# Kernel tuning notes

Measured on AMD Instinct MI355X. Metric: run time of the kernel, lower is better.

## Reference

```python
import jax, jax.numpy as jnp
import numpy as np

R = 2          # candidate_radius
TEMP = 0.1     # temperature
MIN_E = 3
MAX_E = 8      # max_edges_per_node
EPS = 1e-6


def _neighbors(H, W, r):
    # grid neighbor indices (N,K) and relative positions (K,2), clamped at borders
    ys, xs = np.meshgrid(np.arange(H), np.arange(W), indexing='ij')
    idx_grid = ys * W + xs
    nbrs, rel = [], []
    for dy in range(-r, r + 1):
        for dx in range(-r, r + 1):
            if dy == 0 and dx == 0:
                continue
            ny = np.clip(ys + dy, 0, H - 1)
            nx = np.clip(xs + dx, 0, W - 1)
            nbrs.append(idx_grid[ny, nx].ravel())
            rel.append([dx / r, dy / r])
    return jnp.asarray(np.stack(nbrs, 1)), jnp.asarray(np.array(rel, np.float32))


def setup_inputs() -> dict:
    key = jax.random.key(0)
    ks = jax.random.split(key, 12)
    B, C, H, W = 2, 64, 128, 128
    hid = 64
    ein = 2 * C + 2  # edge scorer input dim
    s = 0.05
    return {
        'x':  jax.random.normal(ks[0], (B, C, H, W), jnp.float32),
        'W1': jax.random.normal(ks[1], (hid, ein), jnp.float32) * s,
        'b1': jnp.zeros((hid,), jnp.float32),
        'W2': jax.random.normal(ks[2], (hid // 2, hid), jnp.float32) * s,
        'b2': jnp.zeros((hid // 2,), jnp.float32),
        'W3': jax.random.normal(ks[3], (1, hid // 2), jnp.float32) * s,
        'b3': jnp.zeros((1,), jnp.float32),
        'thr': jnp.asarray(0.0, jnp.float32),
        'Wm': jax.random.normal(ks[4], (C, C), jnp.float32) * s,
        'bm': jnp.zeros((C,), jnp.float32),
        'Wo': jax.random.normal(ks[5], (C, C), jnp.float32) * s,
        'bo': jnp.zeros((C,), jnp.float32),
    }


def reference(x, W1, b1, W2, b2, W3, b3, thr, Wm, bm, Wo, bo):
    B, C, H, W = x.shape
    N = H * W
    nbr, rel = _neighbors(H, W, R)          # (N,K), (K,2)
    K = nbr.shape[1]

    nodes = x.transpose(0, 2, 3, 1).reshape(B, N, C)   # (B,N,C)
    h_tgt = jnp.take(nodes, nbr, axis=1)               # (B,N,K,C) gather neighbors

    # edge scorer layer1: split W1 over [h_src | h_tgt | rel_pos] to avoid (B,N,K,2C+2) concat
    z_src = nodes @ W1[:, :C].T                        # (B,N,hid)
    z_tgt = h_tgt @ W1[:, C:2 * C].T                   # (B,N,K,hid)
    z_pos = rel @ W1[:, 2 * C:].T                      # (K,hid)
    h1 = jax.nn.relu(z_src[:, :, None, :] + z_tgt + z_pos[None, None] + b1)
    h2 = jax.nn.relu(h1 @ W2.T + b2)
    edge_scores = jax.nn.sigmoid((h2 @ W3.T + b3)[..., 0])   # (B,N,K)

    thr_v = jax.nn.sigmoid(thr)
    keep_prob = jax.nn.sigmoid((edge_scores - thr_v) / TEMP)
    mask_thr = edge_scores >= thr_v
    counts = mask_thr.sum(axis=2)                       # (B,N)

    def topk_mask(k):
        _, idx = jax.lax.top_k(edge_scores, k)          # (B,N,k)
        return jax.nn.one_hot(idx, K, dtype=jnp.float32).sum(-2) > 0

    m_max = topk_mask(min(MAX_E, K))
    m_min = topk_mask(min(MIN_E, K))
    use_max = (counts > MAX_E)[..., None]
    use_min = (counts < MIN_E)[..., None]
    use_t = ~use_max & ~use_min
    final_mask = (use_max & m_max) | (use_min & m_min) | (use_t & mask_thr)

    msgs = jax.nn.relu(h_tgt @ Wm.T + bm)               # (B,N,K,C)
    w = (edge_scores * keep_prob * final_mask.astype(edge_scores.dtype))[..., None]
    agg = (msgs * w).sum(axis=2) / (w.sum(axis=2) + EPS)  # (B,N,C)

    out = nodes + agg @ Wo.T + bo
    return out.reshape(B, H, W, C).transpose(0, 3, 1, 2)
```

## Files before the change

kernel.cpp:

```cpp
#include <hip/hip_runtime.h>
#include <hip/hip_bf16.h>
#include <math.h>

#define NNODES 16384
#define KE 24

typedef float f32x4 __attribute__((ext_vector_type(4)));
typedef unsigned u32x4 __attribute__((ext_vector_type(4)));
typedef __fp16 half2_t __attribute__((ext_vector_type(2)));
typedef _Float16 half8_t __attribute__((ext_vector_type(8)));

union fragcast { u32x4 u; half8_t h; half2_t h2[4]; };

__global__ void aux_k(const float* __restrict__ W1, const float* __restrict__ Wm,
                      float* __restrict__ zpos, float* __restrict__ wt)
{
    int t = threadIdx.x;
    for (int idx = t; idx < KE * 64; idx += 256) {
        int k = idx >> 6, h = idx & 63;
        int kk = k + (k >= 12 ? 1 : 0);
        int q5 = (kk * 52) >> 8;
        int dy = q5 - 2;
        int dx = kk - 5 * q5 - 2;
        zpos[idx] = W1[h * 130 + 128] * (dx * 0.5f)
                  + W1[h * 130 + 129] * (dy * 0.5f);
    }
    for (int idx = t; idx < 3 * 64 * 64; idx += 256) {
        int mat = idx >> 12;
        int r = idx & 4095;
        int c = r >> 6, h = r & 63;
        float v = (mat == 0) ? W1[h * 130 + c]
                : (mat == 1) ? W1[h * 130 + 64 + c]
                             : Wm[h * 64 + c];
        wt[idx] = v;
    }
}

__global__ __launch_bounds__(256) void precompute_k(
    const float* __restrict__ x, const float* __restrict__ wt,
    const float* __restrict__ b1, const float* __restrict__ bm,
    float* __restrict__ zsrc, float* __restrict__ ztgt, float* __restrict__ msg)
{
    __shared__ float xt[64][128];
    __shared__ float wl[64][64];
    const int t = threadIdx.x;
    const int mat = blockIdx.x >> 8;
    const int tile = blockIdx.x & 255;
    const int n0 = tile * 128;
    const int b = n0 >> 14;
    const int nl0 = n0 & (NNODES - 1);
    const float* xb = x + (size_t)b * 64 * NNODES + nl0;

    #pragma unroll
    for (int r = 0; r < 8; ++r) {
        int idx = r * 256 + t;
        int c = idx >> 5, j4 = idx & 31;
        float4 v = *(const float4*)(xb + (size_t)c * NNODES + j4 * 4);
        *(float4*)&xt[c][j4 * 4] = v;
    }
    #pragma unroll
    for (int r = 0; r < 4; ++r) {
        int idx = r * 256 + t;
        ((float4*)&wl[0][0])[idx] = ((const float4*)(wt + mat * 4096))[idx];
    }
    __syncthreads();

    const int i = t >> 5;
    const int j = t & 31;

    float acc[8][4];
    #pragma unroll
    for (int a = 0; a < 8; ++a)
        #pragma unroll
        for (int bb = 0; bb < 4; ++bb) acc[a][bb] = 0.f;

    #pragma unroll 4
    for (int c = 0; c < 64; ++c) {
        float4 w0 = *(const float4*)&wl[c][i * 8];
        float4 w1 = *(const float4*)&wl[c][i * 8 + 4];
        float4 x0 = *(const float4*)&xt[c][j * 4];
        float wv[8] = {w0.x, w0.y, w0.z, w0.w, w1.x, w1.y, w1.z, w1.w};
        float xv[4] = {x0.x, x0.y, x0.z, x0.w};
        #pragma unroll
        for (int a = 0; a < 8; ++a)
            #pragma unroll
            for (int bb = 0; bb < 4; ++bb)
                acc[a][bb] = fmaf(wv[a], xv[bb], acc[a][bb]);
    }

    #pragma unroll
    for (int a = 0; a < 8; ++a) {
        float bv = (mat == 0) ? b1[i * 8 + a] : (mat == 2) ? bm[i * 8 + a] : 0.f;
        #pragma unroll
        for (int bb = 0; bb < 4; ++bb) {
            float v = acc[a][bb] + bv;
            acc[a][bb] = (mat == 2) ? fmaxf(v, 0.f) : v;
        }
    }

    float* dst = (mat == 0) ? zsrc : (mat == 1) ? ztgt : msg;
    #pragma unroll
    for (int bb = 0; bb < 4; ++bb) {
        float* o = dst + (size_t)(n0 + j * 4 + bb) * 64 + i * 8;
        *(float4*)o       = make_float4(acc[0][bb], acc[1][bb], acc[2][bb], acc[3][bb]);
        *(float4*)(o + 4) = make_float4(acc[4][bb], acc[5][bb], acc[6][bb], acc[7][bb]);
    }
}

__global__ __launch_bounds__(256, 3) void score_k(
    const float* __restrict__ zsrc, const float* __restrict__ ztgt,
    const float* __restrict__ zpos, const float* __restrict__ W2,
    const float* __restrict__ b2, const float* __restrict__ W3,
    const float* __restrict__ b3, float* __restrict__ scores)
{
    __shared__ fragcast fraglds[64 * 13];
    __shared__ float zpl[24 * 68];

    const int t = threadIdx.x;
    const int l = t & 63;
    const int lcol = l & 15;
    const int lgrp = l >> 4;
    const int w = t >> 6;
    const int wave = blockIdx.x * 4 + w;

    #pragma unroll
    for (int r = 0; r < 6; ++r) {
        int idx = r * 256 + t;
        zpl[(idx >> 6) * 68 + (idx & 63)] = zpos[idx];
    }
    {
        const int jt = w >> 1, kt = w & 1;
        fragcast fh, fl;
        const float* wr = W2 + (size_t)(jt * 16 + lcol) * 64 + kt * 32 + lgrp * 8;
        #pragma unroll
        for (int d = 0; d < 4; ++d) {
            float e0 = wr[2 * d] * 64.f;
            float e1 = wr[2 * d + 1] * 64.f;
            half2_t hh = __builtin_amdgcn_cvt_pkrtz(e0, e1);
            float r0 = e0 - (float)hh[0];
            float r1 = e1 - (float)hh[1];
            fh.h2[d] = hh;
            fl.h2[d] = __builtin_amdgcn_cvt_pkrtz(r0, r1);
        }
        fraglds[l * 13 + 0 + jt * 2 + kt] = fh;
        fraglds[l * 13 + 4 + jt * 2 + kt] = fl;
    }
    __syncthreads();

    const fragcast* fb = &fraglds[l * 13];
    const f32x4 b2l0 = *(const f32x4*)(b2 + lgrp * 4);
    const f32x4 b2l1 = *(const f32x4*)(b2 + 16 + lgrp * 4);
    const f32x4 w3l0 = *(const f32x4*)(W3 + lgrp * 4);
    const f32x4 w3l1 = *(const f32x4*)(W3 + 16 + lgrp * 4);
    const float b3s = b3[0];

    const int node0 = wave * 2;

    #pragma unroll
    for (int Mt = 0; Mt < 3; ++Mt) {
        const int ke = Mt * 16 + lcol;
        const int nsel = (ke >= 24) ? 1 : 0;
        const int node = node0 + nsel;
        const int k = ke - 24 * nsel;
        const int bb = node >> 14;
        const int nl = node & (NNODES - 1);
        const int yy = nl >> 7, xx = nl & 127;
        const int kk = k + (k >= 12 ? 1 : 0);
        const int q5 = (kk * 52) >> 8;
        const int dy = q5 - 2, dx = kk - 5 * q5 - 2;
        const int ny = min(max(yy + dy, 0), 127);
        const int nx = min(max(xx + dx, 0), 127);
        const int nbn = (bb << 14) + (ny << 7) + nx;

        const float* zs = zsrc + (size_t)node * 64 + lgrp * 8;
        const float* zt = ztgt + (size_t)nbn * 64 + lgrp * 8;
        const float* zp = &zpl[k * 68 + lgrp * 8];

        f32x4 ac0A = {0.f,0.f,0.f,0.f}, ac0B = {0.f,0.f,0.f,0.f};
        f32x4 ac1A = {0.f,0.f,0.f,0.f}, ac1B = {0.f,0.f,0.f,0.f};

        #pragma unroll
        for (int kt = 0; kt < 2; ++kt) {
            const int o = kt * 32;
            float4 a0 = *(const float4*)(zs + o);
            float4 a1 = *(const float4*)(zs + o + 4);
            float4 t0 = *(const float4*)(zt + o);
            float4 t1 = *(const float4*)(zt + o + 4);
            float4 p0 = *(const float4*)(zp + o);
            float4 p1 = *(const float4*)(zp + o + 4);
            float v[8];
            v[0] = fmaxf(a0.x + t0.x + p0.x, 0.f);
            v[1] = fmaxf(a0.y + t0.y + p0.y, 0.f);
            v[2] = fmaxf(a0.z + t0.z + p0.z, 0.f);
            v[3] = fmaxf(a0.w + t0.w + p0.w, 0.f);
            v[4] = fmaxf(a1.x + t1.x + p1.x, 0.f);
            v[5] = fmaxf(a1.y + t1.y + p1.y, 0.f);
            v[6] = fmaxf(a1.z + t1.z + p1.z, 0.f);
            v[7] = fmaxf(a1.w + t1.w + p1.w, 0.f);

            fragcast Bh, Bl;
            #pragma unroll
            for (int d = 0; d < 4; ++d) {
                float e0 = v[2 * d], e1 = v[2 * d + 1];
                half2_t hh = __builtin_amdgcn_cvt_pkrtz(e0, e1);
                float r0 = e0 - (float)hh[0];
                float r1 = e1 - (float)hh[1];
                Bh.h2[d] = hh;
                Bl.h2[d] = __builtin_amdgcn_cvt_pkrtz(r0, r1);
            }

            ac0A = __builtin_amdgcn_mfma_f32_16x16x32_f16(fb[0 + kt].h, Bh.h, ac0A, 0, 0, 0);
            ac1A = __builtin_amdgcn_mfma_f32_16x16x32_f16(fb[2 + kt].h, Bh.h, ac1A, 0, 0, 0);
            ac0B = __builtin_amdgcn_mfma_f32_16x16x32_f16(fb[4 + kt].h, Bh.h, ac0B, 0, 0, 0);
            ac1B = __builtin_amdgcn_mfma_f32_16x16x32_f16(fb[6 + kt].h, Bh.h, ac1B, 0, 0, 0);
            ac0B = __builtin_amdgcn_mfma_f32_16x16x32_f16(fb[0 + kt].h, Bl.h, ac0B, 0, 0, 0);
            ac1B = __builtin_amdgcn_mfma_f32_16x16x32_f16(fb[2 + kt].h, Bl.h, ac1B, 0, 0, 0);
        }

        const f32x4 s0 = ac0A + ac0B;
        const f32x4 s1 = ac1A + ac1B;
        float sacc = 0.f;
        #pragma unroll
        for (int q = 0; q < 4; ++q) {
            sacc = fmaf(fmaxf(fmaf(s0[q], 0.015625f, b2l0[q]), 0.f), w3l0[q], sacc);
            sacc = fmaf(fmaxf(fmaf(s1[q], 0.015625f, b2l1[q]), 0.f), w3l1[q], sacc);
        }
        sacc += __shfl_xor(sacc, 16);
        sacc += __shfl_xor(sacc, 32);
        float sig = 1.f / (1.f + expf(-(sacc + b3s)));
        if (l < 16)
            scores[(size_t)node0 * 24 + Mt * 16 + l] = sig;
    }
}

__global__ __launch_bounds__(256) void agg_k(
    const float* __restrict__ x, const float* __restrict__ scores,
    const float* __restrict__ msg, const float* __restrict__ Wo,
    const float* __restrict__ bo, const float* __restrict__ thrp,
    float* __restrict__ out)
{
    __shared__ float sc[768];
    __shared__ float wl[768];
    __shared__ float sumw[32];
    __shared__ float aggL[32][64];
    __shared__ float ot[64][33];

    const int t = threadIdx.x;
    const int n0 = blockIdx.x * 32;
    const int b = n0 >> 14;
    const int nl0 = n0 & (NNODES - 1);
    const float thr_v = 1.f / (1.f + expf(-thrp[0]));

    #pragma unroll
    for (int rep = 0; rep < 3; ++rep)
        sc[rep * 256 + t] = scores[(size_t)n0 * 24 + rep * 256 + t];
    __syncthreads();

    #pragma unroll
    for (int rep = 0; rep < 3; ++rep) {
        int e = rep * 256 + t;
        int nl = (int)(((unsigned)(e >> 3) * 171u) >> 9);
        int k = e - nl * 24;
        float s_e = sc[e];
        int rank = 0, cnt = 0;
        #pragma unroll
        for (int j = 0; j < 24; ++j) {
            float sj = sc[nl * 24 + j];
            rank += (sj > s_e || (sj == s_e && j < k)) ? 1 : 0;
            cnt  += (sj >= thr_v) ? 1 : 0;
        }
        bool mask = (cnt > 8) ? (rank < 8)
                  : ((cnt < 3) ? (rank < 3) : (s_e >= thr_v));
        float keep = 1.f / (1.f + expf(-(s_e - thr_v) * 10.f));
        wl[e] = mask ? s_e * keep : 0.f;
    }
    __syncthreads();

    if (t < 32) {
        float s = 0.f;
        #pragma unroll
        for (int k = 0; k < 24; ++k) s += wl[t * 24 + k];
        sumw[t] = s + 1e-6f;
    }
    __syncthreads();

    const int lane = t & 63;
    const int g4 = t >> 6;

    #pragma unroll
    for (int it = 0; it < 8; ++it) {
        int nl = g4 + it * 4;
        int nn = nl0 + nl;
        int yy = nn >> 7, xx = nn & 127;
        float acc = 0.f;
        #pragma unroll
        for (int k = 0; k < 24; ++k) {
            int kk = k + (k >= 12 ? 1 : 0);
            int q5 = (kk * 52) >> 8;
            int dy = q5 - 2, dx = kk - 5 * q5 - 2;
            int ny = min(max(yy + dy, 0), 127);
            int nx = min(max(xx + dx, 0), 127);
            int nb = (b << 14) + (ny << 7) + nx;
            acc = fmaf(wl[nl * 24 + k], msg[(size_t)nb * 64 + lane], acc);
        }
        aggL[nl][lane] = acc / sumw[nl];
    }

    float4 wo[16];
    #pragma unroll
    for (int c4 = 0; c4 < 16; ++c4) wo[c4] = ((const float4*)Wo)[lane * 16 + c4];
    __syncthreads();

    #pragma unroll
    for (int it = 0; it < 8; ++it) {
        int nl = g4 + it * 4;
        const float4* ar = (const float4*)aggL[nl];
        float a0 = 0.f, a1 = 0.f, a2 = 0.f, a3 = 0.f;
        #pragma unroll
        for (int c4 = 0; c4 < 16; ++c4) {
            float4 wv = wo[c4];
            float4 av = ar[c4];
            a0 = fmaf(av.x, wv.x, a0);
            a1 = fmaf(av.y, wv.y, a1);
            a2 = fmaf(av.z, wv.z, a2);
            a3 = fmaf(av.w, wv.w, a3);
        }
        float v = (a0 + a1) + (a2 + a3) + bo[lane]
                + x[(size_t)b * 64 * NNODES + (size_t)lane * NNODES + nl0 + nl];
        ot[lane][nl] = v;
    }
    __syncthreads();

    #pragma unroll
    for (int rep = 0; rep < 2; ++rep) {
        int idx = rep * 256 + t;
        int o = idx >> 3, p = idx & 7;
        float4 v = make_float4(ot[o][4 * p + 0], ot[o][4 * p + 1],
                               ot[o][4 * p + 2], ot[o][4 * p + 3]);
        *(float4*)(out + (size_t)b * 64 * NNODES + (size_t)o * NNODES + nl0 + 4 * p) = v;
    }
}

extern "C" void kernel_launch(void* const* d_in, const int* in_sizes, int n_in,
                              void* d_out, int out_size, void* d_ws, size_t ws_size,
                              hipStream_t stream)
{
    const float* x   = (const float*)d_in[0];
    const float* W1  = (const float*)d_in[1];
    const float* b1  = (const float*)d_in[2];
    const float* W2  = (const float*)d_in[3];
    const float* b2  = (const float*)d_in[4];
    const float* W3  = (const float*)d_in[5];
    const float* b3  = (const float*)d_in[6];
    const float* thr = (const float*)d_in[7];
    const float* Wm  = (const float*)d_in[8];
    const float* bm  = (const float*)d_in[9];
    const float* Wo  = (const float*)d_in[10];
    const float* bo  = (const float*)d_in[11];
    float* out = (float*)d_out;
    float* ws  = (float*)d_ws;

    float* zsrc   = ws;
    float* ztgt   = ws + 2097152;
    float* msg    = ws + 4194304;
    float* scores = ws + 6291456;
    float* zpos   = ws + 7077888;
    float* wt     = ws + 7079424;

    hipLaunchKernelGGL(aux_k, dim3(1), dim3(256), 0, stream, W1, Wm, zpos, wt);
    hipLaunchKernelGGL(precompute_k, dim3(768), dim3(256), 0, stream,
                       x, wt, b1, bm, zsrc, ztgt, msg);
    hipLaunchKernelGGL(score_k, dim3(4096), dim3(256), 0, stream,
                       zsrc, ztgt, zpos, W2, b2, W3, b3, scores);
    hipLaunchKernelGGL(agg_k, dim3(1024), dim3(256), 0, stream,
                       x, scores, msg, Wo, bo, thr, out);
}
```

Before: 97.81 us.

## Fold aux kernel into precompute, prefetch gathers in score_k, relax launch bounds

Result: faster. 90.42 us (-7.5%).

```diff
diff --git a/kernel.cpp b/kernel.cpp
--- a/kernel.cpp
+++ b/kernel.cpp
@@ -12,34 +12,12 @@
 
 union fragcast { u32x4 u; half8_t h; half2_t h2[4]; };
 
-__global__ void aux_k(const float* __restrict__ W1, const float* __restrict__ Wm,
-                      float* __restrict__ zpos, float* __restrict__ wt)
-{
-    int t = threadIdx.x;
-    for (int idx = t; idx < KE * 64; idx += 256) {
-        int k = idx >> 6, h = idx & 63;
-        int kk = k + (k >= 12 ? 1 : 0);
-        int q5 = (kk * 52) >> 8;
-        int dy = q5 - 2;
-        int dx = kk - 5 * q5 - 2;
-        zpos[idx] = W1[h * 130 + 128] * (dx * 0.5f)
-                  + W1[h * 130 + 129] * (dy * 0.5f);
-    }
-    for (int idx = t; idx < 3 * 64 * 64; idx += 256) {
-        int mat = idx >> 12;
-        int r = idx & 4095;
-        int c = r >> 6, h = r & 63;
-        float v = (mat == 0) ? W1[h * 130 + c]
-                : (mat == 1) ? W1[h * 130 + 64 + c]
-                             : Wm[h * 64 + c];
-        wt[idx] = v;
-    }
-}
-
 __global__ __launch_bounds__(256) void precompute_k(
-    const float* __restrict__ x, const float* __restrict__ wt,
-    const float* __restrict__ b1, const float* __restrict__ bm,
-    float* __restrict__ zsrc, float* __restrict__ ztgt, float* __restrict__ msg)
+    const float* __restrict__ x, const float* __restrict__ W1,
+    const float* __restrict__ Wm, const float* __restrict__ b1,
+    const float* __restrict__ bm,
+    float* __restrict__ zsrc, float* __restrict__ ztgt, float* __restrict__ msg,
+    float* __restrict__ zpos)
 {
     __shared__ float xt[64][128];
     __shared__ float wl[64][64];
@@ -51,6 +29,17 @@
     const int nl0 = n0 & (NNODES - 1);
     const float* xb = x + (size_t)b * 64 * NNODES + nl0;
 
+    if (blockIdx.x == 0) {
+        for (int idx = t; idx < KE * 64; idx += 256) {
+            int k = idx >> 6, h = idx & 63;
+            int kk = k + (k >= 12 ? 1 : 0);
+            int q5 = (kk * 52) >> 8;
+            int dy = q5 - 2, dx = kk - 5 * q5 - 2;
+            zpos[idx] = W1[h * 130 + 128] * (dx * 0.5f)
+                      + W1[h * 130 + 129] * (dy * 0.5f);
+        }
+    }
+
     #pragma unroll
     for (int r = 0; r < 8; ++r) {
         int idx = r * 256 + t;
@@ -59,9 +48,13 @@
         *(float4*)&xt[c][j4 * 4] = v;
     }
     #pragma unroll
-    for (int r = 0; r < 4; ++r) {
+    for (int r = 0; r < 16; ++r) {
         int idx = r * 256 + t;
-        ((float4*)&wl[0][0])[idx] = ((const float4*)(wt + mat * 4096))[idx];
+        int c = idx >> 6, h = idx & 63;
+        float v = (mat == 0) ? W1[h * 130 + c]
+                : (mat == 1) ? W1[h * 130 + 64 + c]
+                             : Wm[h * 64 + c];
+        (&wl[0][0])[idx] = v;
     }
     __syncthreads();
 
@@ -107,7 +100,7 @@
     }
 }
 
-__global__ __launch_bounds__(256, 3) void score_k(
+__global__ __launch_bounds__(256, 1) void score_k(
     const float* __restrict__ zsrc, const float* __restrict__ ztgt,
     const float* __restrict__ zpos, const float* __restrict__ W2,
     const float* __restrict__ b2, const float* __restrict__ W3,
@@ -156,6 +149,8 @@
 
     const int node0 = wave * 2;
 
+    int kArr[3];
+    float4 zsv[3][4], ztv[3][4];
     #pragma unroll
     for (int Mt = 0; Mt < 3; ++Mt) {
         const int ke = Mt * 16 + lcol;
@@ -171,23 +166,32 @@
         const int ny = min(max(yy + dy, 0), 127);
         const int nx = min(max(xx + dx, 0), 127);
         const int nbn = (bb << 14) + (ny << 7) + nx;
-
+        kArr[Mt] = k;
         const float* zs = zsrc + (size_t)node * 64 + lgrp * 8;
         const float* zt = ztgt + (size_t)nbn * 64 + lgrp * 8;
-        const float* zp = &zpl[k * 68 + lgrp * 8];
+        zsv[Mt][0] = *(const float4*)(zs);
+        zsv[Mt][1] = *(const float4*)(zs + 4);
+        zsv[Mt][2] = *(const float4*)(zs + 32);
+        zsv[Mt][3] = *(const float4*)(zs + 36);
+        ztv[Mt][0] = *(const float4*)(zt);
+        ztv[Mt][1] = *(const float4*)(zt + 4);
+        ztv[Mt][2] = *(const float4*)(zt + 32);
+        ztv[Mt][3] = *(const float4*)(zt + 36);
+    }
+
+    #pragma unroll
+    for (int Mt = 0; Mt < 3; ++Mt) {
+        const float* zp = &zpl[kArr[Mt] * 68 + lgrp * 8];
 
         f32x4 ac0A = {0.f,0.f,0.f,0.f}, ac0B = {0.f,0.f,0.f,0.f};
         f32x4 ac1A = {0.f,0.f,0.f,0.f}, ac1B = {0.f,0.f,0.f,0.f};
 
         #pragma unroll
         for (int kt = 0; kt < 2; ++kt) {
-            const int o = kt * 32;
-            float4 a0 = *(const float4*)(zs + o);
-            float4 a1 = *(const float4*)(zs + o + 4);
-            float4 t0 = *(const float4*)(zt + o);
-            float4 t1 = *(const float4*)(zt + o + 4);
-            float4 p0 = *(const float4*)(zp + o);
-            float4 p1 = *(const float4*)(zp + o + 4);
+            float4 a0 = zsv[Mt][2 * kt], a1 = zsv[Mt][2 * kt + 1];
+            float4 t0 = ztv[Mt][2 * kt], t1 = ztv[Mt][2 * kt + 1];
+            float4 p0 = *(const float4*)(zp + kt * 32);
+            float4 p1 = *(const float4*)(zp + kt * 32 + 4);
             float v[8];
             v[0] = fmaxf(a0.x + t0.x + p0.x, 0.f);
             v[1] = fmaxf(a0.y + t0.y + p0.y, 0.f);
@@ -365,11 +369,9 @@
     float* msg    = ws + 4194304;
     float* scores = ws + 6291456;
     float* zpos   = ws + 7077888;
-    float* wt     = ws + 7079424;
-
-    hipLaunchKernelGGL(aux_k, dim3(1), dim3(256), 0, stream, W1, Wm, zpos, wt);
+
     hipLaunchKernelGGL(precompute_k, dim3(768), dim3(256), 0, stream,
-                       x, wt, b1, bm, zsrc, ztgt, msg);
+                       x, W1, Wm, b1, bm, zsrc, ztgt, msg, zpos);
     hipLaunchKernelGGL(score_k, dim3(4096), dim3(256), 0, stream,
                        zsrc, ztgt, zpos, W2, b2, W3, b3, scores);
     hipLaunchKernelGGL(agg_k, dim3(1024), dim3(256), 0, stream,
```
